# Optimization experiments

Measured on AMD Instinct MI355X. Metric: run time of the kernel, lower is better.

Reference implementation:

```python
import jax, jax.numpy as jnp
import numpy as np

B = 8          # graphs (FOVs)
NPG = 16384    # clusters per graph
N = B * NPG
K = 6          # knn k=5+1, loop=True
E = N * K
C0PG = 2048    # superclusters_0 per graph
C0 = B * C0PG
C1PG = 256     # superclusters_1 per graph
C1 = B * C1PG
L = 10         # 4 cluster-level + 3 SC0 + 3 SC1 PointTransformerConv layers
D = 64


def setup_inputs() -> dict:
    key = jax.random.key(0)
    ks = jax.random.split(key, 20)
    s = 0.05  # weight scale for stable attention logits
    x = jax.random.normal(ks[0], (N, D), jnp.float32)
    pos_c = jax.random.uniform(ks[1], (N, 2), jnp.float32)
    dst_c = jnp.repeat(jnp.arange(N, dtype=jnp.int32), K)
    src_c = jax.random.randint(ks[2], (E,), 0, N, jnp.int32)
    src_c = src_c.at[::K].set(jnp.arange(N, dtype=jnp.int32))  # self-loops
    batch = (jnp.arange(N, dtype=jnp.int32) // NPG)
    sc_id0 = (jnp.arange(N, dtype=jnp.int32) % C0PG)   # every SC0 id present per graph
    pos_sc0 = jax.random.uniform(ks[3], (C0, 2), jnp.float32)
    sc_id1 = (jnp.arange(C0, dtype=jnp.int32) % C1PG)
    pos_sc1 = jax.random.uniform(ks[4], (C1, 2), jnp.float32)
    return dict(
        x=x, pos_c=pos_c, src_c=src_c, dst_c=dst_c, batch=batch,
        sc_id0=sc_id0, pos_sc0=pos_sc0, sc_id1=sc_id1, pos_sc1=pos_sc1,
        Wlin=jax.random.normal(ks[5], (L, D, D)) * s,
        Wsrc=jax.random.normal(ks[6], (L, D, D)) * s,
        Wdst=jax.random.normal(ks[7], (L, D, D)) * s,
        pW1=jax.random.normal(ks[8], (L, 2, D)) * s,
        pB1=jnp.zeros((L, D), jnp.float32),
        pW2=jax.random.normal(ks[9], (L, D, D)) * s,
        pB2=jnp.zeros((L, D), jnp.float32),
        aW1=jax.random.normal(ks[10], (L, D, D)) * s,
        aB1=jnp.zeros((L, D), jnp.float32),
        aW2=jax.random.normal(ks[11], (L, D, D)) * s,
        aB2=jnp.zeros((L, D), jnp.float32),
        head_w=jax.random.normal(ks[12], (D, 2)) * s,
        head_b=jnp.zeros((2,), jnp.float32),
    )


def mlp2(x, W1, b1, W2, b2):
    # PyG MLP(plain_last=False): Linear->ReLU twice (eval mode, BN at init = identity)
    h = jax.nn.relu(x @ W1 + b1)
    return jax.nn.relu(h @ W2 + b2)


def ptconv(h, pos, src, dst, n, p, l):
    # PointTransformerConv: delta = pos_nn(pos_i - pos_j);
    # alpha = softmax_i(attn_nn(lin_dst(x)_i - lin_src(x)_j + delta));
    # out_i = max_j alpha * (lin(x)_j + delta)
    xv = h @ p['Wlin'][l]
    a_src = h @ p['Wsrc'][l]
    a_dst = h @ p['Wdst'][l]
    delta = mlp2(pos[dst] - pos[src], p['pW1'][l], p['pB1'][l], p['pW2'][l], p['pB2'][l])
    a = mlp2(a_dst[dst] - a_src[src] + delta, p['aW1'][l], p['aB1'][l], p['aW2'][l], p['aB2'][l])
    m = jax.ops.segment_max(a, dst, num_segments=n)
    e = jnp.exp(a - m[dst])
    ssum = jax.ops.segment_sum(e, dst, num_segments=n)
    alpha = e / ssum[dst]
    return jax.ops.segment_max(alpha * (xv[src] + delta), dst, num_segments=n)


def gen_cluster(ids, batch, nb):
    mx = jax.ops.segment_max(ids, batch, num_segments=nb)
    off = jnp.cumsum(jnp.concatenate([jnp.zeros((1,), ids.dtype), mx + 1]))
    return ids + off[batch].astype(ids.dtype)


def knn_edges(pos, b, npg, k):
    # knn_graph(k, loop=True) per graph: src=neighbor, dst=center
    p = pos.reshape(b, npg, 2)
    sq = jnp.sum(p * p, axis=-1)
    d2 = sq[:, :, None] + sq[:, None, :] - 2.0 * jnp.einsum('bnd,bmd->bnm', p, p)
    idx = jax.lax.top_k(-d2, k)[1]  # [b, npg, k], includes self (d=0)
    src = (idx + (jnp.arange(b) * npg)[:, None, None]).reshape(-1).astype(jnp.int32)
    dst = jnp.repeat(jnp.arange(b * npg, dtype=jnp.int32), k)
    return src, dst


def reference(x, pos_c, src_c, dst_c, batch, sc_id0, pos_sc0, sc_id1, pos_sc1,
              Wlin, Wsrc, Wdst, pW1, pB1, pW2, pB2, aW1, aB1, aW2, aB2,
              head_w, head_b):
    p = dict(Wlin=Wlin, Wsrc=Wsrc, Wdst=Wdst, pW1=pW1, pB1=pB1, pW2=pW2, pB2=pB2,
             aW1=aW1, aB1=aB1, aW2=aW2, aB2=aB2)
    h = x
    for l in range(4):  # cluster_encoder_0..3 on clusters graph
        h = ptconv(h, pos_c, src_c, dst_c, N, p, l)
    # pool clusters -> superclusters_0
    cl0 = gen_cluster(sc_id0, batch, B)
    h0 = jax.ops.segment_max(h, cl0, num_segments=C0)
    batch0 = jax.ops.segment_max(batch, cl0, num_segments=C0)
    src0, dst0 = knn_edges(pos_sc0, B, C0PG, K)
    for l in range(4, 7):
        h0 = ptconv(h0, pos_sc0, src0, dst0, C0, p, l)
    # pool SC0 -> superclusters_1
    cl1 = gen_cluster(sc_id1, batch0, B)
    h1 = jax.ops.segment_max(h0, cl1, num_segments=C1)
    batch1 = jax.ops.segment_max(batch0, cl1, num_segments=C1)
    src1, dst1 = knn_edges(pos_sc1, B, C1PG, K)
    for l in range(7, 10):
        h1 = ptconv(h1, pos_sc1, src1, dst1, C1, p, l)
    g = jax.ops.segment_max(h1, batch1, num_segments=B)  # global_max_pool
    return g @ head_w + head_b
```

## Files before the change

### kernel.cpp

```cpp
#include <hip/hip_runtime.h>
#include <cstdint>

namespace {
constexpr int BG   = 8;
constexpr int NPG  = 16384;
constexpr int NN   = BG * NPG;
constexpr int KK   = 6;
constexpr int C0PG = 2048;
constexpr int C0N  = BG * C0PG;
constexpr int C1PG = 256;
constexpr int C1N  = BG * C1PG;
constexpr int D    = 64;
constexpr int SEG0 = C0PG / 256;
constexpr int VS   = 198;
constexpr int NMS  = 132;
}

__device__ __forceinline__ unsigned f2u_ord(float v) {
  unsigned u = __float_as_uint(v);
  return (u & 0x80000000u) ? ~u : (u | 0x80000000u);
}

__global__ void k_init_u32(unsigned* __restrict__ p, unsigned v, int n) {
  int i = blockIdx.x * blockDim.x + threadIdx.x;
  if (i < n) p[i] = v;
}

__global__ void k_seg_max_i32(const int* __restrict__ vals, const int* __restrict__ seg,
                              int* __restrict__ out, int n) {
  int i = blockIdx.x * blockDim.x + threadIdx.x;
  if (i < n) atomicMax(&out[seg[i]], vals[i]);
}

template <int NB>
__global__ __launch_bounds__(256) void k_seg_max_small(
    const int* __restrict__ vals, const int* __restrict__ seg,
    int* __restrict__ out, int n) {
  __shared__ int lmx[NB];
  int t = threadIdx.x;
  if (t < NB) lmx[t] = (int)0x80000000;
  __syncthreads();
  for (int i = blockIdx.x * 256 + t; i < n; i += gridDim.x * 256)
    atomicMax(&lmx[seg[i]], vals[i]);
  __syncthreads();
  if (t < NB) atomicMax(&out[t], lmx[t]);
}

__global__ void k_cumsum_off(const int* __restrict__ mx, int* __restrict__ off, int nb) {
  if (threadIdx.x == 0 && blockIdx.x == 0) {
    int a = 0; off[0] = 0;
    for (int b = 0; b < nb; ++b) { a += mx[b] + 1; off[b + 1] = a; }
  }
}

__global__ void k_gen_cl(const int* __restrict__ ids, const int* __restrict__ bt,
                         const int* __restrict__ off, int* __restrict__ cl, int n) {
  int i = blockIdx.x * blockDim.x + threadIdx.x;
  if (i < n) cl[i] = ids[i] + off[bt[i]];
}

__global__ void k_pool_f32(const float* __restrict__ h, const int* __restrict__ cl,
                           unsigned* __restrict__ outu, int total) {
  int i = blockIdx.x * blockDim.x + threadIdx.x;
  if (i < total) atomicMax(&outu[(size_t)cl[i >> 6] * D + (i & 63)], f2u_ord(h[i]));
}

__global__ void k_decode_f32(unsigned* __restrict__ p, int n) {
  int i = blockIdx.x * blockDim.x + threadIdx.x;
  if (i < n) { unsigned u = p[i]; p[i] = (u & 0x80000000u) ? (u ^ 0x80000000u) : ~u; }
}

__global__ __launch_bounds__(256) void k_knn(const float* __restrict__ pos, int npg,
                                             int* __restrict__ srcOut) {
  #pragma clang fp contract(off)
  __shared__ float px[2048], py[2048], sq[2048];
  int t = threadIdx.x;
  int nglob = blockIdx.x * 256 + t;
  int graph = nglob / npg;
  int base = graph * npg;
  for (int i = t; i < npg; i += 256) {
    float xx = pos[2 * (base + i)];
    float yy = pos[2 * (base + i) + 1];
    px[i] = xx; py[i] = yy;
    float a = xx * xx; float b = yy * yy;
    sq[i] = a + b;
  }
  __syncthreads();
  int i = nglob - base;
  float xi = px[i], yi = py[i], sqi = sq[i];
  float bd[KK]; int bi[KK];
  #pragma unroll
  for (int q = 0; q < KK; ++q) { bd[q] = 3.4e38f; bi[q] = 0; }
  for (int j = 0; j < npg; ++j) {
    float t1 = xi * px[j];
    float t2 = yi * py[j];
    float dot = t1 + t2;
    float d2 = (sqi + sq[j]) - 2.0f * dot;
    if (d2 < bd[KK - 1]) {
      bd[KK - 1] = d2; bi[KK - 1] = j;
      #pragma unroll
      for (int q = KK - 1; q > 0; --q) {
        if (bd[q] < bd[q - 1]) {
          float td = bd[q]; bd[q] = bd[q - 1]; bd[q - 1] = td;
          int ti = bi[q]; bi[q] = bi[q - 1]; bi[q - 1] = ti;
        }
      }
    }
  }
  #pragma unroll
  for (int q = 0; q < KK; ++q) srcOut[(size_t)nglob * KK + q] = base + bi[q];
}

__global__ __launch_bounds__(256) void k_knn_part(const float* __restrict__ pos, int npg,
                                                  int nseg,
                                                  float* __restrict__ outD,
                                                  int* __restrict__ outI) {
  #pragma clang fp contract(off)
  __shared__ float cx[256], cy[256], cs[256];
  int t = threadIdx.x;
  int qt = blockIdx.x / nseg;
  int s  = blockIdx.x % nseg;
  int qlo = qt * 256;
  int graph = qlo / npg;
  int base = graph * npg;
  int cbase = base + s * 256;
  {
    float xx = pos[2 * (cbase + t)];
    float yy = pos[2 * (cbase + t) + 1];
    cx[t] = xx; cy[t] = yy;
    float a = xx * xx; float b = yy * yy;
    cs[t] = a + b;
  }
  __syncthreads();
  int q = qlo + t;
  float xi = pos[2 * q], yi = pos[2 * q + 1];
  float qa = xi * xi; float qb = yi * yi;
  float sqi = qa + qb;
  float bd[KK]; int bi[KK];
  #pragma unroll
  for (int u = 0; u < KK; ++u) { bd[u] = 3.4e38f; bi[u] = 0; }
  for (int j = 0; j < 256; ++j) {
    float t1 = xi * cx[j];
    float t2 = yi * cy[j];
    float dot = t1 + t2;
    float d2 = (sqi + cs[j]) - 2.0f * dot;
    if (d2 < bd[KK - 1]) {
      bd[KK - 1] = d2; bi[KK - 1] = cbase + j;
      #pragma unroll
      for (int u = KK - 1; u > 0; --u) {
        if (bd[u] < bd[u - 1]) {
          float td = bd[u]; bd[u] = bd[u - 1]; bd[u - 1] = td;
          int ti = bi[u]; bi[u] = bi[u - 1]; bi[u - 1] = ti;
        }
      }
    }
  }
  size_t ob = (size_t)q * (nseg * KK) + (size_t)s * KK;
  #pragma unroll
  for (int u = 0; u < KK; ++u) { outD[ob + u] = bd[u]; outI[ob + u] = bi[u]; }
}

__global__ void k_knn_merge(const float* __restrict__ inD, const int* __restrict__ inI,
                            int nseg, int* __restrict__ srcOut, int nq) {
  int q = blockIdx.x * blockDim.x + threadIdx.x;
  if (q >= nq) return;
  float bd[KK]; int bi[KK];
  #pragma unroll
  for (int u = 0; u < KK; ++u) { bd[u] = 3.4e38f; bi[u] = 0x7fffffff; }
  size_t ib = (size_t)q * (nseg * KK);
  for (int e = 0; e < nseg * KK; ++e) {
    float d = inD[ib + e]; int ix = inI[ib + e];
    bool lt = (d < bd[KK - 1]) || (d == bd[KK - 1] && ix < bi[KK - 1]);
    if (lt) {
      bd[KK - 1] = d; bi[KK - 1] = ix;
      #pragma unroll
      for (int u = KK - 1; u > 0; --u) {
        bool sw = (bd[u] < bd[u - 1]) || (bd[u] == bd[u - 1] && bi[u] < bi[u - 1]);
        if (sw) {
          float td = bd[u]; bd[u] = bd[u - 1]; bd[u - 1] = td;
          int ti = bi[u]; bi[u] = bi[u - 1]; bi[u - 1] = ti;
        }
      }
    }
  }
  #pragma unroll
  for (int u = 0; u < KK; ++u) srcOut[(size_t)q * KK + u] = bi[u];
}

__global__ __launch_bounds__(256, 4) void k_node_mm(const float* __restrict__ hin,
    const float* __restrict__ Wl, const float* __restrict__ Ws, const float* __restrict__ Wd,
    float* __restrict__ xv, float* __restrict__ as_, float* __restrict__ ad_) {
  __shared__ float wbuf[2048];
  __shared__ float vbuf[32 * NMS];
  int t = threadIdx.x;
  size_t nb = (size_t)blockIdx.x * 128;
  int ng = t >> 3, cb = t & 7, c0 = cb * 8;
  const float* Wm[3] = {Wl, Ws, Wd};
  float* Om[3] = {xv, as_, ad_};
  const float4* h4 = (const float4*)hin;
  float acc[3][32];
  #pragma unroll
  for (int m = 0; m < 3; ++m)
    #pragma unroll
    for (int i = 0; i < 32; ++i) acc[m][i] = 0.0f;
  for (int kh = 0; kh < 2; ++kh) {
    #pragma unroll
    for (int r = 0; r < 4; ++r) {
      int flat = r * 256 + t;
      int n = flat >> 3, kq = flat & 7;
      float4 hv = h4[(nb + n) * 16 + kh * 8 + kq];
      vbuf[(kq * 4 + 0) * NMS + n] = hv.x;
      vbuf[(kq * 4 + 1) * NMS + n] = hv.y;
      vbuf[(kq * 4 + 2) * NMS + n] = hv.z;
      vbuf[(kq * 4 + 3) * NMS + n] = hv.w;
    }
    #pragma unroll
    for (int m = 0; m < 3; ++m) {
      {
        const float4* w4 = (const float4*)Wm[m] + kh * 512;
        float4* wb = (float4*)wbuf;
        wb[t] = w4[t];
        wb[256 + t] = w4[256 + t];
      }
      __syncthreads();
      #pragma clang loop unroll_count(2)
      for (int kk = 0; kk < 32; ++kk) {
        float4 v4 = *(const float4*)&vbuf[kk * NMS + 4 * ng];
        float4 w0 = *(const float4*)&wbuf[kk * 64 + c0];
        float4 w1 = *(const float4*)&wbuf[kk * 64 + c0 + 4];
        float vv[4] = {v4.x, v4.y, v4.z, v4.w};
        float wv[8] = {w0.x, w0.y, w0.z, w0.w, w1.x, w1.y, w1.z, w1.w};
        #pragma unroll
        for (int ni = 0; ni < 4; ++ni)
          #pragma unroll
          for (int c = 0; c < 8; ++c)
            acc[m][ni * 8 + c] = fmaf(vv[ni], wv[c], acc[m][ni * 8 + c]);
      }
      __syncthreads();
    }
  }
  #pragma unroll
  for (int m = 0; m < 3; ++m) {
    float* O = Om[m];
    #pragma unroll
    for (int ni = 0; ni < 4; ++ni) {
      *(float4*)(O + (nb + 4 * ng + ni) * 64 + c0) =
          make_float4(acc[m][ni * 8 + 0], acc[m][ni * 8 + 1],
                      acc[m][ni * 8 + 2], acc[m][ni * 8 + 3]);
      *(float4*)(O + (nb + 4 * ng + ni) * 64 + c0 + 4) =
          make_float4(acc[m][ni * 8 + 4], acc[m][ni * 8 + 5],
                      acc[m][ni * 8 + 6], acc[m][ni * 8 + 7]);
    }
  }
}

__global__ __launch_bounds__(256, 4) void k_edge_fused(
    const float* __restrict__ pos, const int* __restrict__ srcA,
    const float* __restrict__ as_, const float* __restrict__ ad_,
    const float* __restrict__ xv,
    const float* __restrict__ pW1, const float* __restrict__ pB1,
    const float* __restrict__ pW2, const float* __restrict__ pB2,
    const float* __restrict__ aW1, const float* __restrict__ aB1,
    const float* __restrict__ aW2, const float* __restrict__ aB2,
    float* __restrict__ hout) {
  __shared__ float wbuf[2048];
  __shared__ float vbuf[32 * VS];
  __shared__ float sbuf[192];
  __shared__ float pdxs[192], pdys[192];
  __shared__ int   srcb[192];
  int t = threadIdx.x;
  int nb = blockIdx.x * 32;
  int ng = t >> 3;
  int cb = t & 7;
  int cl = 4 * cb;
  int ch = 32 + 4 * cb;
  int node = nb + ng;

  if (t < 192) {
    int s = srcA[(size_t)nb * KK + t];
    srcb[t] = s;
    int dn = nb + t / KK;
    float2 pd = *(const float2*)(pos + 2 * (size_t)dn);
    float2 ps = *(const float2*)(pos + 2 * (size_t)s);
    pdxs[t] = pd.x - ps.x;
    pdys[t] = pd.y - ps.y;
    sbuf[t] = (t < 128) ? pW1[t] : pB1[t - 128];
  }
  __syncthreads();

  float d[48];
  {
    float4 b0 = *(const float4*)(pB2 + cl);
    float4 b1 = *(const float4*)(pB2 + ch);
    #pragma unroll
    for (int j = 0; j < 6; ++j) {
      d[j * 8 + 0] = b0.x; d[j * 8 + 1] = b0.y; d[j * 8 + 2] = b0.z; d[j * 8 + 3] = b0.w;
      d[j * 8 + 4] = b1.x; d[j * 8 + 5] = b1.y; d[j * 8 + 6] = b1.z; d[j * 8 + 7] = b1.w;
    }
  }
  #pragma unroll
  for (int h = 0; h < 2; ++h) {
    {
      const float4* w4 = (const float4*)pW2 + h * 512;
      float4* wb = (float4*)wbuf;
      wb[t] = w4[t];
      wb[256 + t] = w4[256 + t];
    }
    if (t < 192) {
      float px = pdxs[t], py = pdys[t];
      #pragma clang loop unroll_count(4)
      for (int kk = 0; kk < 32; ++kk) {
        int k = h * 32 + kk;
        float p0 = px * sbuf[k];
        float p1 = py * sbuf[64 + k];
        float ph = fmaxf((p0 + p1) + sbuf[128 + k], 0.0f);
        vbuf[kk * VS + t] = ph;
      }
    }
    __syncthreads();
    #pragma clang loop unroll_count(2)
    for (int kk = 0; kk < 32; ++kk) {
      float2 v01 = *(const float2*)&vbuf[kk * VS + 6 * ng];
      float2 v23 = *(const float2*)&vbuf[kk * VS + 6 * ng + 2];
      float2 v45 = *(const float2*)&vbuf[kk * VS + 6 * ng + 4];
      float4 w0 = *(const float4*)&wbuf[kk * 64 + cl];
      float4 w1 = *(const float4*)&wbuf[kk * 64 + ch];
      float vv[6] = {v01.x, v01.y, v23.x, v23.y, v45.x, v45.y};
      float wv[8] = {w0.x, w0.y, w0.z, w0.w, w1.x, w1.y, w1.z, w1.w};
      #pragma unroll
      for (int j = 0; j < 6; ++j)
        #pragma unroll
        for (int c = 0; c < 8; ++c)
          d[j * 8 + c] = fmaf(vv[j], wv[c], d[j * 8 + c]);
    }
    __syncthreads();
  }
  #pragma unroll
  for (int i = 0; i < 48; ++i) d[i] = fmaxf(d[i], 0.0f);

  float r[48];
  {
    float4 b0 = *(const float4*)(aB1 + cl);
    float4 b1 = *(const float4*)(aB1 + ch);
    #pragma unroll
    for (int j = 0; j < 6; ++j) {
      r[j * 8 + 0] = b0.x; r[j * 8 + 1] = b0.y; r[j * 8 + 2] = b0.z; r[j * 8 + 3] = b0.w;
      r[j * 8 + 4] = b1.x; r[j * 8 + 5] = b1.y; r[j * 8 + 6] = b1.z; r[j * 8 + 7] = b1.w;
    }
  }
  #pragma unroll
  for (int h = 0; h < 2; ++h) {
    {
      const float4* w4 = (const float4*)aW1 + h * 512;
      float4* wb = (float4*)wbuf;
      wb[t] = w4[t];
      wb[256 + t] = w4[256 + t];
    }
    {
      int cbase = h ? ch : cl;
      float4 av = *(const float4*)(ad_ + (size_t)node * 64 + cbase);
      float vtmp[6][4];
      #pragma unroll
      for (int j = 0; j < 6; ++j) {
        int s = srcb[6 * ng + j];
        float4 sv = *(const float4*)(as_ + (size_t)s * 64 + cbase);
        vtmp[j][0] = (av.x - sv.x) + d[j * 8 + 4 * h + 0];
        vtmp[j][1] = (av.y - sv.y) + d[j * 8 + 4 * h + 1];
        vtmp[j][2] = (av.z - sv.z) + d[j * 8 + 4 * h + 2];
        vtmp[j][3] = (av.w - sv.w) + d[j * 8 + 4 * h + 3];
      }
      #pragma unroll
      for (int cj = 0; cj < 4; ++cj)
        #pragma unroll
        for (int jp = 0; jp < 3; ++jp)
          *(float2*)&vbuf[(4 * cb + cj) * VS + 6 * ng + 2 * jp] =
              make_float2(vtmp[2 * jp][cj], vtmp[2 * jp + 1][cj]);
    }
    __syncthreads();
    #pragma clang loop unroll_count(2)
    for (int kk = 0; kk < 32; ++kk) {
      float2 v01 = *(const float2*)&vbuf[kk * VS + 6 * ng];
      float2 v23 = *(const float2*)&vbuf[kk * VS + 6 * ng + 2];
      float2 v45 = *(const float2*)&vbuf[kk * VS + 6 * ng + 4];
      float4 w0 = *(const float4*)&wbuf[kk * 64 + cl];
      float4 w1 = *(const float4*)&wbuf[kk * 64 + ch];
      float vv[6] = {v01.x, v01.y, v23.x, v23.y, v45.x, v45.y};
      float wv[8] = {w0.x, w0.y, w0.z, w0.w, w1.x, w1.y, w1.z, w1.w};
      #pragma unroll
      for (int j = 0; j < 6; ++j)
        #pragma unroll
        for (int c = 0; c < 8; ++c)
          r[j * 8 + c] = fmaf(vv[j], wv[c], r[j * 8 + c]);
    }
    __syncthreads();
  }
  #pragma unroll
  for (int i = 0; i < 48; ++i) r[i] = fmaxf(r[i], 0.0f);

  float a[48];
  {
    float4 b0 = *(const float4*)(aB2 + cl);
    float4 b1 = *(const float4*)(aB2 + ch);
    #pragma unroll
    for (int j = 0; j < 6; ++j) {
      a[j * 8 + 0] = b0.x; a[j * 8 + 1] = b0.y; a[j * 8 + 2] = b0.z; a[j * 8 + 3] = b0.w;
      a[j * 8 + 4] = b1.x; a[j * 8 + 5] = b1.y; a[j * 8 + 6] = b1.z; a[j * 8 + 7] = b1.w;
    }
  }
  #pragma unroll
  for (int h = 0; h < 2; ++h) {
    {
      const float4* w4 = (const float4*)aW2 + h * 512;
      float4* wb = (float4*)wbuf;
      wb[t] = w4[t];
      wb[256 + t] = w4[256 + t];
    }
    #pragma unroll
    for (int cj = 0; cj < 4; ++cj)
      #pragma unroll
      for (int jp = 0; jp < 3; ++jp)
        *(float2*)&vbuf[(4 * cb + cj) * VS + 6 * ng + 2 * jp] =
            make_float2(r[(2 * jp) * 8 + 4 * h + cj], r[(2 * jp + 1) * 8 + 4 * h + cj]);
    __syncthreads();
    #pragma clang loop unroll_count(2)
    for (int kk = 0; kk < 32; ++kk) {
      float2 v01 = *(const float2*)&vbuf[kk * VS + 6 * ng];
      float2 v23 = *(const float2*)&vbuf[kk * VS + 6 * ng + 2];
      float2 v45 = *(const float2*)&vbuf[kk * VS + 6 * ng + 4];
      float4 w0 = *(const float4*)&wbuf[kk * 64 + cl];
      float4 w1 = *(const float4*)&wbuf[kk * 64 + ch];
      float vv[6] = {v01.x, v01.y, v23.x, v23.y, v45.x, v45.y};
      float wv[8] = {w0.x, w0.y, w0.z, w0.w, w1.x, w1.y, w1.z, w1.w};
      #pragma unroll
      for (int j = 0; j < 6; ++j)
        #pragma unroll
        for (int c = 0; c < 8; ++c)
          a[j * 8 + c] = fmaf(vv[j], wv[c], a[j * 8 + c]);
    }
    __syncthreads();
  }
  #pragma unroll
  for (int i = 0; i < 48; ++i) a[i] = fmaxf(a[i], 0.0f);

  float m8[8], ss[8], out[8];
  #pragma unroll
  for (int c = 0; c < 8; ++c) m8[c] = a[c];
  #pragma unroll
  for (int j = 1; j < 6; ++j)
    #pragma unroll
    for (int c = 0; c < 8; ++c) m8[c] = fmaxf(m8[c], a[j * 8 + c]);
  #pragma unroll
  for (int c = 0; c < 8; ++c) ss[c] = 0.0f;
  #pragma unroll
  for (int j = 0; j < 6; ++j)
    #pragma unroll
    for (int c = 0; c < 8; ++c) ss[c] += expf(a[j * 8 + c] - m8[c]);
  #pragma unroll
  for (int j = 0; j < 6; ++j) {
    int s = srcb[6 * ng + j];
    float4 x0 = *(const float4*)(xv + (size_t)s * 64 + cl);
    float4 x1 = *(const float4*)(xv + (size_t)s * 64 + ch);
    float xa[8] = {x0.x, x0.y, x0.z, x0.w, x1.x, x1.y, x1.z, x1.w};
    #pragma unroll
    for (int c = 0; c < 8; ++c) {
      float ej = expf(a[j * 8 + c] - m8[c]);
      float alpha = ej / ss[c];
      float val = alpha * (xa[c] + d[j * 8 + c]);
      out[c] = (j == 0) ? val : fmaxf(out[c], val);
    }
  }
  *(float4*)(hout + (size_t)node * 64 + cl) = make_float4(out[0], out[1], out[2], out[3]);
  *(float4*)(hout + (size_t)node * 64 + ch) = make_float4(out[4], out[5], out[6], out[7]);
}

__global__ void k_head(const float* __restrict__ g, const float* __restrict__ hw,
                       const float* __restrict__ hb, float* __restrict__ out) {
  int t = threadIdx.x;
  if (t >= BG * 2) return;
  int b = t >> 1, o = t & 1;
  float acc = 0.0f;
  for (int k = 0; k < D; ++k) acc = fmaf(g[b * D + k], hw[k * 2 + o], acc);
  out[b * 2 + o] = acc + hb[o];
}

extern "C" void kernel_launch(void* const* d_in, const int* in_sizes, int n_in,
                              void* d_out, int out_size, void* d_ws, size_t ws_size,
                              hipStream_t stream) {
  (void)in_sizes; (void)n_in; (void)out_size; (void)ws_size;
  const float* x      = (const float*)d_in[0];
  const float* pos_c  = (const float*)d_in[1];
  const int*   src_c  = (const int*)d_in[2];
  const int*   batch  = (const int*)d_in[4];
  const int*   sc_id0 = (const int*)d_in[5];
  const float* pos_s0 = (const float*)d_in[6];
  const int*   sc_id1 = (const int*)d_in[7];
  const float* pos_s1 = (const float*)d_in[8];
  const float* Wlin = (const float*)d_in[9];
  const float* Wsrc = (const float*)d_in[10];
  const float* Wdst = (const float*)d_in[11];
  const float* pW1  = (const float*)d_in[12];
  const float* pB1  = (const float*)d_in[13];
  const float* pW2  = (const float*)d_in[14];
  const float* pB2  = (const float*)d_in[15];
  const float* aW1  = (const float*)d_in[16];
  const float* aB1  = (const float*)d_in[17];
  const float* aW2  = (const float*)d_in[18];
  const float* aB2  = (const float*)d_in[19];
  const float* hw   = (const float*)d_in[20];
  const float* hb   = (const float*)d_in[21];
  float* outp = (float*)d_out;

  char* ws = (char*)d_ws;
  size_t off = 0;
  auto alloc = [&](size_t bytes) -> void* {
    void* p = ws + off; off = (off + bytes + 255) & ~(size_t)255; return p;
  };
  float* h   = (float*)alloc((size_t)NN * D * 4);
  float* xv  = (float*)alloc((size_t)NN * D * 4);
  float* as_ = (float*)alloc((size_t)NN * D * 4);
  float* ad_ = (float*)alloc((size_t)NN * D * 4);
  float* h0  = (float*)alloc((size_t)C0N * D * 4);
  float* h1  = (float*)alloc((size_t)C1N * D * 4);
  float* g   = (float*)alloc((size_t)BG * D * 4);
  int* cl0   = (int*)alloc((size_t)NN * 4);
  int* cl1   = (int*)alloc((size_t)C0N * 4);
  int* b0    = (int*)alloc((size_t)C0N * 4);
  int* b1    = (int*)alloc((size_t)C1N * 4);
  int* src0  = (int*)alloc((size_t)C0N * KK * 4);
  int* src1  = (int*)alloc((size_t)C1N * KK * 4);
  float* kd  = (float*)alloc((size_t)C0N * SEG0 * KK * 4);
  int*   ki  = (int*)alloc((size_t)C0N * SEG0 * KK * 4);
  int* mx    = (int*)alloc(256);
  int* offb  = (int*)alloc(256);

  auto ptconv = [&](int n, const float* pos, const int* srcA,
                    const float* hin, float* hout, int l) {
    k_node_mm<<<n / 128, 256, 0, stream>>>(hin,
        Wlin + (size_t)l * 4096, Wsrc + (size_t)l * 4096, Wdst + (size_t)l * 4096,
        xv, as_, ad_);
    k_edge_fused<<<n / 32, 256, 0, stream>>>(pos, srcA, as_, ad_, xv,
        pW1 + (size_t)l * 128, pB1 + (size_t)l * 64,
        pW2 + (size_t)l * 4096, pB2 + (size_t)l * 64,
        aW1 + (size_t)l * 4096, aB1 + (size_t)l * 64,
        aW2 + (size_t)l * 4096, aB2 + (size_t)l * 64,
        hout);
  };

  k_init_u32<<<1, 64, 0, stream>>>((unsigned*)mx, 0x80000000u, BG);
  k_seg_max_small<BG><<<64, 256, 0, stream>>>(sc_id0, batch, mx, NN);
  k_cumsum_off<<<1, 1, 0, stream>>>(mx, offb, BG);
  k_gen_cl<<<NN / 256, 256, 0, stream>>>(sc_id0, batch, offb, cl0, NN);
  k_init_u32<<<(C0N + 255) / 256, 256, 0, stream>>>((unsigned*)b0, 0x80000000u, C0N);
  k_seg_max_i32<<<NN / 256, 256, 0, stream>>>(batch, cl0, b0, NN);
  k_knn_part<<<(C0N / 256) * SEG0, 256, 0, stream>>>(pos_s0, C0PG, SEG0, kd, ki);
  k_knn_merge<<<C0N / 256, 256, 0, stream>>>(kd, ki, SEG0, src0, C0N);
  k_init_u32<<<1, 64, 0, stream>>>((unsigned*)mx, 0x80000000u, BG);
  k_seg_max_small<BG><<<64, 256, 0, stream>>>(sc_id1, b0, mx, C0N);
  k_cumsum_off<<<1, 1, 0, stream>>>(mx, offb, BG);
  k_gen_cl<<<C0N / 256, 256, 0, stream>>>(sc_id1, b0, offb, cl1, C0N);
  k_init_u32<<<(C1N + 255) / 256, 256, 0, stream>>>((unsigned*)b1, 0x80000000u, C1N);
  k_seg_max_i32<<<C0N / 256, 256, 0, stream>>>(b0, cl1, b1, C0N);
  k_knn<<<C1N / 256, 256, 0, stream>>>(pos_s1, C1PG, src1);

  ptconv(NN, pos_c, src_c, x, h, 0);
  for (int l = 1; l < 4; ++l) ptconv(NN, pos_c, src_c, h, h, l);
  k_init_u32<<<C0N * D / 256, 256, 0, stream>>>((unsigned*)h0, 0x007fffffu, C0N * D);
  k_pool_f32<<<NN * D / 256, 256, 0, stream>>>(h, cl0, (unsigned*)h0, NN * D);
  k_decode_f32<<<C0N * D / 256, 256, 0, stream>>>((unsigned*)h0, C0N * D);
  for (int l = 4; l < 7; ++l) ptconv(C0N, pos_s0, src0, h0, h0, l);
  k_init_u32<<<C1N * D / 256, 256, 0, stream>>>((unsigned*)h1, 0x007fffffu, C1N * D);
  k_pool_f32<<<C0N * D / 256, 256, 0, stream>>>(h0, cl1, (unsigned*)h1, C0N * D);
  k_decode_f32<<<C1N * D / 256, 256, 0, stream>>>((unsigned*)h1, C1N * D);
  for (int l = 7; l < 10; ++l) ptconv(C1N, pos_s1, src1, h1, h1, l);
  k_init_u32<<<(BG * D + 255) / 256, 256, 0, stream>>>((unsigned*)g, 0x007fffffu, BG * D);
  k_pool_f32<<<C1N * D / 256, 256, 0, stream>>>(h1, b1, (unsigned*)g, C1N * D);
  k_decode_f32<<<(BG * D + 255) / 256, 256, 0, stream>>>((unsigned*)g, BG * D);
  k_head<<<1, 64, 0, stream>>>(g, hw, hb, outp);
}
```

Baseline: 1.908 ms.

## Halve nodes per block in edge kernel to cut per-thread register tiles

```diff
diff --git a/kernel.cpp b/kernel.cpp
--- a/kernel.cpp
+++ b/kernel.cpp
@@ -12,7 +12,7 @@
 constexpr int C1N  = BG * C1PG;
 constexpr int D    = 64;
 constexpr int SEG0 = C0PG / 256;
-constexpr int VS   = 198;
+constexpr int VS   = 98;
 constexpr int NMS  = 132;
 }
 
@@ -187,7 +187,9 @@
   for (int u = 0; u < KK; ++u) srcOut[(size_t)q * KK + u] = bi[u];
 }
 
-__global__ __launch_bounds__(256, 4) void k_node_mm(const float* __restrict__ hin,
+__global__ void __launch_bounds__(256)
+__attribute__((amdgpu_waves_per_eu(4, 4)))
+k_node_mm(const float* __restrict__ hin,
     const float* __restrict__ Wl, const float* __restrict__ Ws, const float* __restrict__ Wd,
     float* __restrict__ xv, float* __restrict__ as_, float* __restrict__ ad_) {
   __shared__ float wbuf[2048];
@@ -254,7 +256,9 @@
   }
 }
 
-__global__ __launch_bounds__(256, 4) void k_edge_fused(
+__global__ void __launch_bounds__(256)
+__attribute__((amdgpu_waves_per_eu(4, 4)))
+k_edge_fused(
     const float* __restrict__ pos, const int* __restrict__ srcA,
     const float* __restrict__ as_, const float* __restrict__ ad_,
     const float* __restrict__ xv,
@@ -266,17 +270,17 @@
   __shared__ float wbuf[2048];
   __shared__ float vbuf[32 * VS];
   __shared__ float sbuf[192];
-  __shared__ float pdxs[192], pdys[192];
-  __shared__ int   srcb[192];
+  __shared__ float pdxs[96], pdys[96];
+  __shared__ int   srcb[96];
   int t = threadIdx.x;
-  int nb = blockIdx.x * 32;
-  int ng = t >> 3;
-  int cb = t & 7;
-  int cl = 4 * cb;
-  int ch = 32 + 4 * cb;
+  int nb = blockIdx.x * 16;
+  int ng = t >> 4;
+  int cb = t & 15;
+  int cl = 2 * cb;
+  int ch = 32 + 2 * cb;
   int node = nb + ng;
 
-  if (t < 192) {
+  if (t < 96) {
     int s = srcA[(size_t)nb * KK + t];
     srcb[t] = s;
     int dn = nb + t / KK;
@@ -284,18 +288,18 @@
     float2 ps = *(const float2*)(pos + 2 * (size_t)s);
     pdxs[t] = pd.x - ps.x;
     pdys[t] = pd.y - ps.y;
-    sbuf[t] = (t < 128) ? pW1[t] : pB1[t - 128];
-  }
+  }
+  if (t < 192) sbuf[t] = (t < 128) ? pW1[t] : pB1[t - 128];
   __syncthreads();
 
-  float d[48];
+  float d[24];
   {
-    float4 b0 = *(const float4*)(pB2 + cl);
-    float4 b1 = *(const float4*)(pB2 + ch);
+    float2 b0 = *(const float2*)(pB2 + cl);
+    float2 b1 = *(const float2*)(pB2 + ch);
     #pragma unroll
     for (int j = 0; j < 6; ++j) {
-      d[j * 8 + 0] = b0.x; d[j * 8 + 1] = b0.y; d[j * 8 + 2] = b0.z; d[j * 8 + 3] = b0.w;
-      d[j * 8 + 4] = b1.x; d[j * 8 + 5] = b1.y; d[j * 8 + 6] = b1.z; d[j * 8 + 7] = b1.w;
+      d[j * 4 + 0] = b0.x; d[j * 4 + 1] = b0.y;
+      d[j * 4 + 2] = b1.x; d[j * 4 + 3] = b1.y;
     }
   }
   #pragma unroll
@@ -306,7 +310,7 @@
       wb[t] = w4[t];
       wb[256 + t] = w4[256 + t];
     }
-    if (t < 192) {
+    if (t < 96) {
       float px = pdxs[t], py = pdys[t];
       #pragma clang loop unroll_count(4)
       for (int kk = 0; kk < 32; ++kk) {
@@ -323,29 +327,29 @@
       float2 v01 = *(const float2*)&vbuf[kk * VS + 6 * ng];
       float2 v23 = *(const float2*)&vbuf[kk * VS + 6 * ng + 2];
       float2 v45 = *(const float2*)&vbuf[kk * VS + 6 * ng + 4];
-      float4 w0 = *(const float4*)&wbuf[kk * 64 + cl];
-      float4 w1 = *(const float4*)&wbuf[kk * 64 + ch];
+      float2 w0 = *(const float2*)&wbuf[kk * 64 + cl];
+      float2 w1 = *(const float2*)&wbuf[kk * 64 + ch];
       float vv[6] = {v01.x, v01.y, v23.x, v23.y, v45.x, v45.y};
-      float wv[8] = {w0.x, w0.y, w0.z, w0.w, w1.x, w1.y, w1.z, w1.w};
+      float wv[4] = {w0.x, w0.y, w1.x, w1.y};
       #pragma unroll
       for (int j = 0; j < 6; ++j)
         #pragma unroll
-        for (int c = 0; c < 8; ++c)
-          d[j * 8 + c] = fmaf(vv[j], wv[c], d[j * 8 + c]);
+        for (int c = 0; c < 4; ++c)
+          d[j * 4 + c] = fmaf(vv[j], wv[c], d[j * 4 + c]);
     }
     __syncthreads();
   }
   #pragma unroll
-  for (int i = 0; i < 48; ++i) d[i] = fmaxf(d[i], 0.0f);
-
-  float r[48];
+  for (int i = 0; i < 24; ++i) d[i] = fmaxf(d[i], 0.0f);
+
+  float r[24];
   {
-    float4 b0 = *(const float4*)(aB1 + cl);
-    float4 b1 = *(const float4*)(aB1 + ch);
+    float2 b0 = *(const float2*)(aB1 + cl);
+    float2 b1 = *(const float2*)(aB1 + ch);
     #pragma unroll
     for (int j = 0; j < 6; ++j) {
-      r[j * 8 + 0] = b0.x; r[j * 8 + 1] = b0.y; r[j * 8 + 2] = b0.z; r[j * 8 + 3] = b0.w;
-      r[j * 8 + 4] = b1.x; r[j * 8 + 5] = b1.y; r[j * 8 + 6] = b1.z; r[j * 8 + 7] = b1.w;
+      r[j * 4 + 0] = b0.x; r[j * 4 + 1] = b0.y;
+      r[j * 4 + 2] = b1.x; r[j * 4 + 3] = b1.y;
     }
   }
   #pragma unroll
@@ -358,23 +362,20 @@
     }
     {
       int cbase = h ? ch : cl;
-      float4 av = *(const float4*)(ad_ + (size_t)node * 64 + cbase);
-      float vtmp[6][4];
+      float2 av = *(const float2*)(ad_ + (size_t)node * 64 + cbase);
+      float v0[6], v1[6];
       #pragma unroll
       for (int j = 0; j < 6; ++j) {
         int s = srcb[6 * ng + j];
-        float4 sv = *(const float4*)(as_ + (size_t)s * 64 + cbase);
-        vtmp[j][0] = (av.x - sv.x) + d[j * 8 + 4 * h + 0];
-        vtmp[j][1] = (av.y - sv.y) + d[j * 8 + 4 * h + 1];
-        vtmp[j][2] = (av.z - sv.z) + d[j * 8 + 4 * h + 2];
-        vtmp[j][3] = (av.w - sv.w) + d[j * 8 + 4 * h + 3];
-      }
-      #pragma unroll
-      for (int cj = 0; cj < 4; ++cj)
-        #pragma unroll
-        for (int jp = 0; jp < 3; ++jp)
-          *(float2*)&vbuf[(4 * cb + cj) * VS + 6 * ng + 2 * jp] =
-              make_float2(vtmp[2 * jp][cj], vtmp[2 * jp + 1][cj]);
+        float2 sv = *(const float2*)(as_ + (size_t)s * 64 + cbase);
+        v0[j] = (av.x - sv.x) + d[j * 4 + 2 * h + 0];
+        v1[j] = (av.y - sv.y) + d[j * 4 + 2 * h + 1];
+      }
+      #pragma unroll
+      for (int jp = 0; jp < 3; ++jp) {
+        *(float2*)&vbuf[(cl + 0) * VS + 6 * ng + 2 * jp] = make_float2(v0[2 * jp], v0[2 * jp + 1]);
+        *(float2*)&vbuf[(cl + 1) * VS + 6 * ng + 2 * jp] = make_float2(v1[2 * jp], v1[2 * jp + 1]);
+      }
     }
     __syncthreads();
     #pragma clang loop unroll_count(2)
@@ -382,29 +383,29 @@
       float2 v01 = *(const float2*)&vbuf[kk * VS + 6 * ng];
       float2 v23 = *(const float2*)&vbuf[kk * VS + 6 * ng + 2];
       float2 v45 = *(const float2*)&vbuf[kk * VS + 6 * ng + 4];
-      float4 w0 = *(const float4*)&wbuf[kk * 64 + cl];
-      float4 w1 = *(const float4*)&wbuf[kk * 64 + ch];
+      float2 w0 = *(const float2*)&wbuf[kk * 64 + cl];
+      float2 w1 = *(const float2*)&wbuf[kk * 64 + ch];
       float vv[6] = {v01.x, v01.y, v23.x, v23.y, v45.x, v45.y};
-      float wv[8] = {w0.x, w0.y, w0.z, w0.w, w1.x, w1.y, w1.z, w1.w};
+      float wv[4] = {w0.x, w0.y, w1.x, w1.y};
       #pragma unroll
       for (int j = 0; j < 6; ++j)
         #pragma unroll
-        for (int c = 0; c < 8; ++c)
-          r[j * 8 + c] = fmaf(vv[j], wv[c], r[j * 8 + c]);
+        for (int c = 0; c < 4; ++c)
+          r[j * 4 + c] = fmaf(vv[j], wv[c], r[j * 4 + c]);
     }
     __syncthreads();
   }
   #pragma unroll
-  for (int i = 0; i < 48; ++i) r[i] = fmaxf(r[i], 0.0f);
-
-  float a[48];
+  for (int i = 0; i < 24; ++i) r[i] = fmaxf(r[i], 0.0f);
+
+  float a[24];
   {
-    float4 b0 = *(const float4*)(aB2 + cl);
-    float4 b1 = *(const float4*)(aB2 + ch);
+    float2 b0 = *(const float2*)(aB2 + cl);
+    float2 b1 = *(const float2*)(aB2 + ch);
     #pragma unroll
     for (int j = 0; j < 6; ++j) {
-      a[j * 8 + 0] = b0.x; a[j * 8 + 1] = b0.y; a[j * 8 + 2] = b0.z; a[j * 8 + 3] = b0.w;
-      a[j * 8 + 4] = b1.x; a[j * 8 + 5] = b1.y; a[j * 8 + 6] = b1.z; a[j * 8 + 7] = b1.w;
+      a[j * 4 + 0] = b0.x; a[j * 4 + 1] = b0.y;
+      a[j * 4 + 2] = b1.x; a[j * 4 + 3] = b1.y;
     }
   }
   #pragma unroll
@@ -416,61 +417,62 @@
       wb[256 + t] = w4[256 + t];
     }
     #pragma unroll
-    for (int cj = 0; cj < 4; ++cj)
-      #pragma unroll
-      for (int jp = 0; jp < 3; ++jp)
-        *(float2*)&vbuf[(4 * cb + cj) * VS + 6 * ng + 2 * jp] =
-            make_float2(r[(2 * jp) * 8 + 4 * h + cj], r[(2 * jp + 1) * 8 + 4 * h + cj]);
+    for (int jp = 0; jp < 3; ++jp) {
+      *(float2*)&vbuf[(cl + 0) * VS + 6 * ng + 2 * jp] =
+          make_float2(r[(2 * jp) * 4 + 2 * h + 0], r[(2 * jp + 1) * 4 + 2 * h + 0]);
+      *(float2*)&vbuf[(cl + 1) * VS + 6 * ng + 2 * jp] =
+          make_float2(r[(2 * jp) * 4 + 2 * h + 1], r[(2 * jp + 1) * 4 + 2 * h + 1]);
+    }
     __syncthreads();
     #pragma clang loop unroll_count(2)
     for (int kk = 0; kk < 32; ++kk) {
       float2 v01 = *(const float2*)&vbuf[kk * VS + 6 * ng];
       float2 v23 = *(const float2*)&vbuf[kk * VS + 6 * ng + 2];
       float2 v45 = *(const float2*)&vbuf[kk * VS + 6 * ng + 4];
-      float4 w0 = *(const float4*)&wbuf[kk * 64 + cl];
-      float4 w1 = *(const float4*)&wbuf[kk * 64 + ch];
+      float2 w0 = *(const float2*)&wbuf[kk * 64 + cl];
+      float2 w1 = *(const float2*)&wbuf[kk * 64 + ch];
       float vv[6] = {v01.x, v01.y, v23.x, v23.y, v45.x, v45.y};
-      float wv[8] = {w0.x, w0.y, w0.z, w0.w, w1.x, w1.y, w1.z, w1.w};
+      float wv[4] = {w0.x, w0.y, w1.x, w1.y};
       #pragma unroll
       for (int j = 0; j < 6; ++j)
         #pragma unroll
-        for (int c = 0; c < 8; ++c)
-          a[j * 8 + c] = fmaf(vv[j], wv[c], a[j * 8 + c]);
+        for (int c = 0; c < 4; ++c)
+          a[j * 4 + c] = fmaf(vv[j], wv[c], a[j * 4 + c]);
     }
     __syncthreads();
   }
   #pragma unroll
-  for (int i = 0; i < 48; ++i) a[i] = fmaxf(a[i], 0.0f);
-
-  float m8[8], ss[8], out[8];
-  #pragma unroll
-  for (int c = 0; c < 8; ++c) m8[c] = a[c];
+  for (int i = 0; i < 24; ++i) a[i] = fmaxf(a[i], 0.0f);
+
+  float m4[4], ss[4], out[4];
+  #pragma unroll
+  for (int c = 0; c < 4; ++c) m4[c] = a[c];
   #pragma unroll
   for (int j = 1; j < 6; ++j)
     #pragma unroll
-    for (int c = 0; c < 8; ++c) m8[c] = fmaxf(m8[c], a[j * 8 + c]);
-  #pragma unroll
-  for (int c = 0; c < 8; ++c) ss[c] = 0.0f;
+    for (int c = 0; c < 4; ++c) m4[c] = fmaxf(m4[c], a[j * 4 + c]);
+  #pragma unroll
+  for (int c = 0; c < 4; ++c) ss[c] = 0.0f;
   #pragma unroll
   for (int j = 0; j < 6; ++j)
     #pragma unroll
-    for (int c = 0; c < 8; ++c) ss[c] += expf(a[j * 8 + c] - m8[c]);
+    for (int c = 0; c < 4; ++c) ss[c] += expf(a[j * 4 + c] - m4[c]);
   #pragma unroll
   for (int j = 0; j < 6; ++j) {
     int s = srcb[6 * ng + j];
-    float4 x0 = *(const float4*)(xv + (size_t)s * 64 + cl);
-    float4 x1 = *(const float4*)(xv + (size_t)s * 64 + ch);
-    float xa[8] = {x0.x, x0.y, x0.z, x0.w, x1.x, x1.y, x1.z, x1.w};
-    #pragma unroll
-    for (int c = 0; c < 8; ++c) {
-      float ej = expf(a[j * 8 + c] - m8[c]);
+    float2 x0 = *(const float2*)(xv + (size_t)s * 64 + cl);
+    float2 x1 = *(const float2*)(xv + (size_t)s * 64 + ch);
+    float xa[4] = {x0.x, x0.y, x1.x, x1.y};
+    #pragma unroll
+    for (int c = 0; c < 4; ++c) {
+      float ej = expf(a[j * 4 + c] - m4[c]);
       float alpha = ej / ss[c];
-      float val = alpha * (xa[c] + d[j * 8 + c]);
+      float val = alpha * (xa[c] + d[j * 4 + c]);
       out[c] = (j == 0) ? val : fmaxf(out[c], val);
     }
   }
-  *(float4*)(hout + (size_t)node * 64 + cl) = make_float4(out[0], out[1], out[2], out[3]);
-  *(float4*)(hout + (size_t)node * 64 + ch) = make_float4(out[4], out[5], out[6], out[7]);
+  *(float2*)(hout + (size_t)node * 64 + cl) = make_float2(out[0], out[1]);
+  *(float2*)(hout + (size_t)node * 64 + ch) = make_float2(out[2], out[3]);
 }
 
 __global__ void k_head(const float* __restrict__ g, const float* __restrict__ hw,
@@ -538,7 +540,7 @@
     k_node_mm<<<n / 128, 256, 0, stream>>>(hin,
         Wlin + (size_t)l * 4096, Wsrc + (size_t)l * 4096, Wdst + (size_t)l * 4096,
         xv, as_, ad_);
-    k_edge_fused<<<n / 32, 256, 0, stream>>>(pos, srcA, as_, ad_, xv,
+    k_edge_fused<<<n / 16, 256, 0, stream>>>(pos, srcA, as_, ad_, xv,
         pW1 + (size_t)l * 128, pB1 + (size_t)l * 64,
         pW2 + (size_t)l * 4096, pB2 + (size_t)l * 64,
         aW1 + (size_t)l * 4096, aB1 + (size_t)l * 64,
```

After: 2.023 ms. 6.0% more time.
